# Performance work log

Measured on AMD Instinct MI355X. Metric: run time of the kernel, lower is better.

## Reference

```python
import jax, jax.numpy as jnp
import numpy as np

N, E, D_IN, HEADS, C = 100000, 1600000, 128, 4, 32  # C = out_channels per head


def setup_inputs() -> dict:
    key = jax.random.key(0)
    ks = jax.random.split(key, 10)
    s = 1.0 / np.sqrt(D_IN)
    return {
        "x": jax.random.normal(ks[0], (N, D_IN), jnp.float32),
        "edge_index": jax.random.randint(ks[1], (2, E), 0, N, jnp.int64),
        "Wq": jax.random.normal(ks[2], (D_IN, HEADS * C), jnp.float32) * s,
        "bq": jnp.zeros((HEADS * C,), jnp.float32),
        "Wk": jax.random.normal(ks[3], (D_IN, HEADS * C), jnp.float32) * s,
        "bk": jnp.zeros((HEADS * C,), jnp.float32),
        "Wv": jax.random.normal(ks[4], (D_IN, HEADS * C), jnp.float32) * s,
        "bv": jnp.zeros((HEADS * C,), jnp.float32),
        "Wskip": jax.random.normal(ks[5], (D_IN, HEADS * C), jnp.float32) * s,
        "bskip": jnp.zeros((HEADS * C,), jnp.float32),
    }


def reference(x, edge_index, Wq, bq, Wk, bk, Wv, bv, Wskip, bskip):
    n = x.shape[0]
    src, dst = edge_index[0], edge_index[1]  # message flows src (j) -> dst (i)
    q = (x @ Wq + bq).reshape(n, HEADS, C)
    k = (x @ Wk + bk).reshape(n, HEADS, C)
    v = (x @ Wv + bv).reshape(n, HEADS, C)

    # per-edge attention logits [E, H]
    alpha = jnp.einsum('ehc,ehc->eh', q[dst], k[src]) / jnp.sqrt(jnp.float32(C))

    # segment softmax over incoming edges of each target node
    m = jax.ops.segment_max(alpha, dst, num_segments=n)          # [N, H]
    p = jnp.exp(alpha - m[dst])                                   # [E, H]
    z = jax.ops.segment_sum(p, dst, num_segments=n)               # [N, H]
    w = p / (z[dst] + 1e-16)                                      # [E, H]

    # softmax-weighted scatter aggregation of values
    out = jax.ops.segment_sum(v[src] * w[:, :, None], dst, num_segments=n)
    out = out.reshape(n, HEADS * C)

    # root/skip connection (beta=False default: plain add)
    out = out + x @ Wskip + bskip
    return out
```

## Files before the change

### kernel.cpp

```cpp
#include <hip/hip_runtime.h>

#define DIN 128
#define NHEADS 4
#define CH 32
#define MT 128
#define NPB 256
#define EPB_IT 25

#define ST_H 136

typedef _Float16 h8 __attribute__((ext_vector_type(8)));
typedef _Float16 h2 __attribute__((ext_vector_type(2)));
typedef float f4 __attribute__((ext_vector_type(4)));

__global__ __launch_bounds__(256) void prep_w(
    const float* __restrict__ Wq, const float* __restrict__ Wk,
    const float* __restrict__ Wv, const float* __restrict__ Wsk,
    _Float16* __restrict__ wt)
{
    int i = blockIdx.x * 256 + threadIdx.x;
    if (i >= 4 * 16384) return;
    int mat = i >> 14;
    int rem = i & 16383;
    int n  = rem >> 7;
    int kk = rem & 127;
    const float* W = (mat == 0) ? Wq : (mat == 1) ? Wk : (mat == 2) ? Wv : Wsk;
    wt[i] = (_Float16)W[kk * 128 + n];
}

__global__ __launch_bounds__(256) void qkvs_mat(
    const float* __restrict__ x, const _Float16* __restrict__ wt,
    const float* __restrict__ bq, const float* __restrict__ bk,
    const float* __restrict__ bv, const float* __restrict__ bsk,
    _Float16* __restrict__ qh, _Float16* __restrict__ kh,
    _Float16* __restrict__ vh, _Float16* __restrict__ skiph, int N)
{
    __shared__ _Float16 Sbuf[17408];
    const int t = threadIdx.x;
    const int mat = blockIdx.x;
    const int rowBase = blockIdx.y * MT;

    for (int i = t; i < MT * 16; i += 256) {
        int r  = i >> 4;
        int c8 = i & 15;
        int gr = rowBase + r;
        _Float16 h[8];
        if (gr < N) {
            float4 f0 = reinterpret_cast<const float4*>(x)[(size_t)gr * 32 + c8 * 2];
            float4 f1 = reinterpret_cast<const float4*>(x)[(size_t)gr * 32 + c8 * 2 + 1];
            h[0] = (_Float16)f0.x; h[1] = (_Float16)f0.y;
            h[2] = (_Float16)f0.z; h[3] = (_Float16)f0.w;
            h[4] = (_Float16)f1.x; h[5] = (_Float16)f1.y;
            h[6] = (_Float16)f1.z; h[7] = (_Float16)f1.w;
        } else {
            #pragma unroll
            for (int j = 0; j < 8; ++j) h[j] = (_Float16)0.f;
        }
        *reinterpret_cast<uint4*>(&Sbuf[r * 128 + ((c8 ^ (r & 7)) << 3)]) =
            *reinterpret_cast<uint4*>(h);
    }
    __syncthreads();

    const int wid  = t >> 6;
    const int l    = t & 63;
    const int lm   = l & 15;
    const int quad = l >> 4;

    const _Float16* __restrict__ Bsrc = wt + (size_t)mat * 16384;

    f4 acc[2][8];
    #pragma unroll
    for (int ms = 0; ms < 2; ++ms)
        #pragma unroll
        for (int nt = 0; nt < 8; ++nt)
            acc[ms][nt] = (f4){0.f, 0.f, 0.f, 0.f};

    #pragma unroll
    for (int kq = 0; kq < 4; ++kq) {
        const int c8 = kq * 4 + quad;
        const int k0 = c8 << 3;
        h8 a0 = *reinterpret_cast<const h8*>(
            &Sbuf[(wid * 32 + lm) * 128 + ((c8 ^ (lm & 7)) << 3)]);
        h8 a1 = *reinterpret_cast<const h8*>(
            &Sbuf[(wid * 32 + 16 + lm) * 128 + ((c8 ^ (lm & 7)) << 3)]);
        #pragma unroll
        for (int nt = 0; nt < 8; ++nt) {
            h8 b = *reinterpret_cast<const h8*>(
                &Bsrc[(size_t)(nt * 16 + lm) * 128 + k0]);
            acc[0][nt] = __builtin_amdgcn_mfma_f32_16x16x32_f16(a0, b, acc[0][nt], 0, 0, 0);
            acc[1][nt] = __builtin_amdgcn_mfma_f32_16x16x32_f16(a1, b, acc[1][nt], 0, 0, 0);
        }
    }
    __syncthreads();

    const float* bias = (mat == 0) ? bq : (mat == 1) ? bk : (mat == 2) ? bv : bsk;

    #pragma unroll
    for (int ms = 0; ms < 2; ++ms) {
        #pragma unroll
        for (int nt = 0; nt < 8; ++nt) {
            int col = nt * 16 + lm;
            float bsv = bias[col];
            int row = wid * 32 + ms * 16 + quad * 4;
            #pragma unroll
            for (int i2 = 0; i2 < 4; ++i2)
                Sbuf[(row + i2) * ST_H + col] = (_Float16)(acc[ms][nt][i2] + bsv);
        }
    }
    __syncthreads();

    _Float16* __restrict__ dst = (mat == 0) ? qh : (mat == 1) ? kh
                               : (mat == 2) ? vh : skiph;
    for (int j = t; j < 2048; j += 256) {
        int r  = j >> 4;
        int c0 = (j & 15) << 3;
        int gr = rowBase + r;
        if (gr < N)
            *reinterpret_cast<uint4*>(&dst[(size_t)gr * 128 + c0]) =
                *reinterpret_cast<const uint4*>(&Sbuf[r * ST_H + c0]);
    }
}

__global__ __launch_bounds__(256) void bucket_hist(
    const int* __restrict__ ei, int* __restrict__ bcnt, int E, int nb)
{
    __shared__ int lds[512];
    for (int b = threadIdx.x; b < nb; b += 256) lds[b] = 0;
    __syncthreads();
    for (long long i = (long long)blockIdx.x * 256 + threadIdx.x; i < E;
         i += (long long)gridDim.x * 256)
        atomicAdd(&lds[ei[(size_t)E + i] >> 8], 1);
    __syncthreads();
    for (int b = threadIdx.x; b < nb; b += 256)
        if (lds[b]) atomicAdd(&bcnt[b], lds[b]);
}

__global__ __launch_bounds__(512) void scan_buckets(
    const int* __restrict__ bcnt, int* __restrict__ boff,
    int* __restrict__ bcur, int nb)
{
    __shared__ int ws[8];
    int t = threadIdx.x, lane = t & 63, wid = t >> 6;
    int v = (t < nb) ? bcnt[t] : 0;
    int s = v;
    #pragma unroll
    for (int off = 1; off < 64; off <<= 1) {
        int n = __shfl_up(s, off);
        if (lane >= off) s += n;
    }
    if (lane == 63) ws[wid] = s;
    __syncthreads();
    int add = 0;
    for (int w = 0; w < wid; ++w) add += ws[w];
    int excl = s - v + add;
    if (t < nb) { boff[t] = excl; bcur[t] = excl; }
    if (t == nb - 1) boff[nb] = excl + v;
}

__global__ __launch_bounds__(256) void bucket_scatter(
    const int* __restrict__ ei, int* __restrict__ bcur,
    unsigned* __restrict__ pairs, int E, int nb)
{
    __shared__ int cnt[512];
    int t = threadIdx.x;
    for (int b = t; b < nb; b += 256) cnt[b] = 0;
    __syncthreads();

    long long e0 = (long long)blockIdx.x * (256 * EPB_IT);
    int ps[EPB_IT], pd[EPB_IT];
    #pragma unroll
    for (int j = 0; j < EPB_IT; ++j) {
        long long e = e0 + j * 256 + t;
        if (e < E) {
            ps[j] = ei[e];
            pd[j] = ei[(size_t)E + e];
            atomicAdd(&cnt[pd[j] >> 8], 1);
        } else pd[j] = -1;
    }
    __syncthreads();
    for (int b = t; b < nb; b += 256) {
        int c = cnt[b];
        if (c) cnt[b] = atomicAdd(&bcur[b], c);
    }
    __syncthreads();
    #pragma unroll
    for (int j = 0; j < EPB_IT; ++j) {
        if (pd[j] >= 0) {
            int pos = atomicAdd(&cnt[pd[j] >> 8], 1);
            pairs[pos] = ((unsigned)ps[j] << 8) | ((unsigned)pd[j] & 255u);
        }
    }
}

__global__ __launch_bounds__(256) void bucket_finalize(
    const unsigned* __restrict__ pairs, const int* __restrict__ boff,
    int* __restrict__ rowptr, int* __restrict__ sorted, int N, int nb)
{
    __shared__ int cnt[NPB];
    __shared__ int cur[NPB];
    __shared__ int ws[4];
    int b = blockIdx.x, t = threadIdx.x;
    cnt[t] = 0;
    __syncthreads();
    int s0 = boff[b], e0 = boff[b + 1];
    for (int i = s0 + t; i < e0; i += 256)
        atomicAdd(&cnt[pairs[i] & (NPB - 1)], 1);
    __syncthreads();

    int v = cnt[t];
    int lane = t & 63, wid = t >> 6;
    int incl = v;
    #pragma unroll
    for (int off = 1; off < 64; off <<= 1) {
        int n = __shfl_up(incl, off);
        if (lane >= off) incl += n;
    }
    if (lane == 63) ws[wid] = incl;
    __syncthreads();
    int add = 0;
    for (int w = 0; w < wid; ++w) add += ws[w];
    int base = s0 + (incl - v) + add;

    int node = b * NPB + t;
    if (node < N) rowptr[node] = base;
    if (b == nb - 1 && t == 0) rowptr[N] = boff[nb];
    cur[t] = base;
    __syncthreads();

    for (int i = s0 + t; i < e0; i += 256) {
        unsigned pr = pairs[i];
        int pos = atomicAdd(&cur[pr & (NPB - 1)], 1);
        sorted[pos] = (int)(pr >> 8);
    }
}

__device__ inline float4 cvt4(unsigned lo, unsigned hi) {
    union { unsigned u[2]; _Float16 h[4]; } c;
    c.u[0] = lo; c.u[1] = hi;
    return make_float4((float)c.h[0], (float)c.h[1], (float)c.h[2], (float)c.h[3]);
}

__device__ inline h2 as_h2(unsigned u) {
    union { unsigned u; h2 h; } c;
    c.u = u;
    return c.h;
}

__global__ __launch_bounds__(256) void node_aggregate(
    const _Float16* __restrict__ q, const _Float16* __restrict__ kh,
    const _Float16* __restrict__ vh, const _Float16* __restrict__ skiph,
    const int* __restrict__ rowptr, const int* __restrict__ srcs,
    float* __restrict__ out, int N)
{
    int gid  = blockIdx.x * 256 + threadIdx.x;
    int node = gid >> 5;
    if (node >= N) return;
    int l = gid & 31;

    uint2 qu = reinterpret_cast<const uint2*>(q + (size_t)node * 128)[l];
    h2 qa = as_h2(qu.x), qb = as_h2(qu.y);

    float4 acc = make_float4(0.f, 0.f, 0.f, 0.f);
    float z = 0.f;

    const uint2* k2 = reinterpret_cast<const uint2*>(kh);
    const uint2* v2 = reinterpret_cast<const uint2*>(vh);
    const float SC = 0.17677669529663687f;
    int e0 = rowptr[node], e1 = rowptr[node + 1];
    int e = e0;

    for (; e + 8 <= e1; e += 8) {
        int s[8];
        #pragma unroll
        for (int j = 0; j < 8; ++j) s[j] = srcs[e + j];
        uint2 kr[8], vr[8];
        #pragma unroll
        for (int j = 0; j < 8; ++j) kr[j] = k2[(size_t)s[j] * 32 + l];
        #pragma unroll
        for (int j = 0; j < 8; ++j) vr[j] = v2[(size_t)s[j] * 32 + l];

        float sv[8];
        #pragma unroll
        for (int j = 0; j < 8; ++j) {
            sv[j] = __builtin_amdgcn_fdot2(qa, as_h2(kr[j].x),
                    __builtin_amdgcn_fdot2(qb, as_h2(kr[j].y), 0.f, false), false);
        }
        #pragma unroll
        for (int j = 0; j < 8; ++j) sv[j] += __shfl_xor(sv[j], 1);
        #pragma unroll
        for (int j = 0; j < 8; ++j) sv[j] += __shfl_xor(sv[j], 2);
        #pragma unroll
        for (int j = 0; j < 8; ++j) sv[j] += __shfl_xor(sv[j], 4);

        #pragma unroll
        for (int j = 0; j < 8; ++j) {
            float p = __expf(sv[j] * SC);
            float4 v = cvt4(vr[j].x, vr[j].y);
            z += p;
            acc.x += p * v.x; acc.y += p * v.y;
            acc.z += p * v.z; acc.w += p * v.w;
        }
    }
    for (; e < e1; ++e) {
        int s0 = srcs[e];
        uint2 kr = k2[(size_t)s0 * 32 + l];
        uint2 vr = v2[(size_t)s0 * 32 + l];
        float sa = __builtin_amdgcn_fdot2(qa, as_h2(kr.x),
                   __builtin_amdgcn_fdot2(qb, as_h2(kr.y), 0.f, false), false);
        sa += __shfl_xor(sa, 1);
        sa += __shfl_xor(sa, 2);
        sa += __shfl_xor(sa, 4);
        float pa = __expf(sa * SC);
        float4 v0 = cvt4(vr.x, vr.y);
        z += pa;
        acc.x += pa * v0.x; acc.y += pa * v0.y;
        acc.z += pa * v0.z; acc.w += pa * v0.w;
    }

    uint2 su = reinterpret_cast<const uint2*>(skiph + (size_t)node * 128)[l];
    float4 sk = cvt4(su.x, su.y);
    float inv = 1.f / (z + 1e-16f);
    float4 o;
    o.x = sk.x + acc.x * inv; o.y = sk.y + acc.y * inv;
    o.z = sk.z + acc.z * inv; o.w = sk.w + acc.w * inv;
    reinterpret_cast<float4*>(out)[(size_t)node * 32 + l] = o;
}

extern "C" void kernel_launch(void* const* d_in, const int* in_sizes, int n_in,
                              void* d_out, int out_size, void* d_ws, size_t ws_size,
                              hipStream_t stream)
{
    const float* x   = (const float*)d_in[0];
    const int*   ei  = (const int*)d_in[1];
    const float* Wq  = (const float*)d_in[2];
    const float* bq  = (const float*)d_in[3];
    const float* Wk  = (const float*)d_in[4];
    const float* bk  = (const float*)d_in[5];
    const float* Wv  = (const float*)d_in[6];
    const float* bv  = (const float*)d_in[7];
    const float* Wsk = (const float*)d_in[8];
    const float* bsk = (const float*)d_in[9];
    float* out = (float*)d_out;

    const int N = in_sizes[0] / DIN;
    const int E = in_sizes[1] / 2;
    const int nb = (N + NPB - 1) / NPB;

    _Float16* qh    = (_Float16*)d_ws;
    _Float16* kh    = qh + (size_t)N * DIN;
    _Float16* vh    = kh + (size_t)N * DIN;
    _Float16* skiph = vh + (size_t)N * DIN;
    _Float16* wt    = skiph + (size_t)N * DIN;
    unsigned* pairs = (unsigned*)(wt + 4 * 16384);
    int* sorted   = (int*)(pairs + (size_t)E);
    int* rowptr   = sorted + E;
    int* bcnt     = rowptr + (N + 1);
    int* boff     = bcnt + 512;
    int* bcur     = boff + 513;

    hipMemsetAsync(bcnt, 0, 512 * sizeof(int), stream);

    prep_w<<<(4 * 16384 + 255) / 256, 256, 0, stream>>>(Wq, Wk, Wv, Wsk, wt);

    dim3 ggrid(4, (N + MT - 1) / MT);
    qkvs_mat<<<ggrid, 256, 0, stream>>>(x, wt, bq, bk, bv, bsk,
                                        qh, kh, vh, skiph, N);

    bucket_hist<<<256, 256, 0, stream>>>(ei, bcnt, E, nb);
    scan_buckets<<<1, 512, 0, stream>>>(bcnt, boff, bcur, nb);
    int sb = (E + 256 * EPB_IT - 1) / (256 * EPB_IT);
    bucket_scatter<<<sb, 256, 0, stream>>>(ei, bcur, pairs, E, nb);
    bucket_finalize<<<nb, 256, 0, stream>>>(pairs, boff, rowptr, sorted, N, nb);

    int ab = (N * 32 + 255) / 256;
    node_aggregate<<<ab, 256, 0, stream>>>(qh, kh, vh, skiph, rowptr, sorted, out, N);
}
```

Measured before the change: 401.9 us.

## Halve GEMM row tile and stage bucket scatter through shared memory

```diff
diff --git a/kernel.cpp b/kernel.cpp
--- a/kernel.cpp
+++ b/kernel.cpp
@@ -3,9 +3,10 @@
 #define DIN 128
 #define NHEADS 4
 #define CH 32
-#define MT 128
+#define MT 64
 #define NPB 256
 #define EPB_IT 25
+#define FB_CAP 6144
 
 #define ST_H 136
 
@@ -35,7 +36,7 @@
     _Float16* __restrict__ qh, _Float16* __restrict__ kh,
     _Float16* __restrict__ vh, _Float16* __restrict__ skiph, int N)
 {
-    __shared__ _Float16 Sbuf[17408];
+    __shared__ _Float16 Sbuf[MT * ST_H];
     const int t = threadIdx.x;
     const int mat = blockIdx.x;
     const int rowBase = blockIdx.y * MT;
@@ -68,27 +69,22 @@
 
     const _Float16* __restrict__ Bsrc = wt + (size_t)mat * 16384;
 
-    f4 acc[2][8];
-    #pragma unroll
-    for (int ms = 0; ms < 2; ++ms)
-        #pragma unroll
-        for (int nt = 0; nt < 8; ++nt)
-            acc[ms][nt] = (f4){0.f, 0.f, 0.f, 0.f};
+    f4 acc[8];
+    #pragma unroll
+    for (int nt = 0; nt < 8; ++nt)
+        acc[nt] = (f4){0.f, 0.f, 0.f, 0.f};
 
     #pragma unroll
     for (int kq = 0; kq < 4; ++kq) {
         const int c8 = kq * 4 + quad;
         const int k0 = c8 << 3;
         h8 a0 = *reinterpret_cast<const h8*>(
-            &Sbuf[(wid * 32 + lm) * 128 + ((c8 ^ (lm & 7)) << 3)]);
-        h8 a1 = *reinterpret_cast<const h8*>(
-            &Sbuf[(wid * 32 + 16 + lm) * 128 + ((c8 ^ (lm & 7)) << 3)]);
+            &Sbuf[(wid * 16 + lm) * 128 + ((c8 ^ (lm & 7)) << 3)]);
         #pragma unroll
         for (int nt = 0; nt < 8; ++nt) {
             h8 b = *reinterpret_cast<const h8*>(
                 &Bsrc[(size_t)(nt * 16 + lm) * 128 + k0]);
-            acc[0][nt] = __builtin_amdgcn_mfma_f32_16x16x32_f16(a0, b, acc[0][nt], 0, 0, 0);
-            acc[1][nt] = __builtin_amdgcn_mfma_f32_16x16x32_f16(a1, b, acc[1][nt], 0, 0, 0);
+            acc[nt] = __builtin_amdgcn_mfma_f32_16x16x32_f16(a0, b, acc[nt], 0, 0, 0);
         }
     }
     __syncthreads();
@@ -96,22 +92,19 @@
     const float* bias = (mat == 0) ? bq : (mat == 1) ? bk : (mat == 2) ? bv : bsk;
 
     #pragma unroll
-    for (int ms = 0; ms < 2; ++ms) {
-        #pragma unroll
-        for (int nt = 0; nt < 8; ++nt) {
-            int col = nt * 16 + lm;
-            float bsv = bias[col];
-            int row = wid * 32 + ms * 16 + quad * 4;
-            #pragma unroll
-            for (int i2 = 0; i2 < 4; ++i2)
-                Sbuf[(row + i2) * ST_H + col] = (_Float16)(acc[ms][nt][i2] + bsv);
-        }
+    for (int nt = 0; nt < 8; ++nt) {
+        int col = nt * 16 + lm;
+        float bsv = bias[col];
+        int row = wid * 16 + quad * 4;
+        #pragma unroll
+        for (int i2 = 0; i2 < 4; ++i2)
+            Sbuf[(row + i2) * ST_H + col] = (_Float16)(acc[nt][i2] + bsv);
     }
     __syncthreads();
 
     _Float16* __restrict__ dst = (mat == 0) ? qh : (mat == 1) ? kh
                                : (mat == 2) ? vh : skiph;
-    for (int j = t; j < 2048; j += 256) {
+    for (int j = t; j < MT * 16; j += 256) {
         int r  = j >> 4;
         int c0 = (j & 15) << 3;
         int gr = rowBase + r;
@@ -199,10 +192,12 @@
     __shared__ int cnt[NPB];
     __shared__ int cur[NPB];
     __shared__ int ws[4];
+    __shared__ int sbuf[FB_CAP];
     int b = blockIdx.x, t = threadIdx.x;
     cnt[t] = 0;
     __syncthreads();
     int s0 = boff[b], e0 = boff[b + 1];
+    int sz = e0 - s0;
     for (int i = s0 + t; i < e0; i += 256)
         atomicAdd(&cnt[pairs[i] & (NPB - 1)], 1);
     __syncthreads();
@@ -219,18 +214,29 @@
     __syncthreads();
     int add = 0;
     for (int w = 0; w < wid; ++w) add += ws[w];
-    int base = s0 + (incl - v) + add;
+    int lbase = (incl - v) + add;
 
     int node = b * NPB + t;
-    if (node < N) rowptr[node] = base;
+    if (node < N) rowptr[node] = s0 + lbase;
     if (b == nb - 1 && t == 0) rowptr[N] = boff[nb];
-    cur[t] = base;
-    __syncthreads();
-
-    for (int i = s0 + t; i < e0; i += 256) {
-        unsigned pr = pairs[i];
-        int pos = atomicAdd(&cur[pr & (NPB - 1)], 1);
-        sorted[pos] = (int)(pr >> 8);
+    cur[t] = lbase;
+    __syncthreads();
+
+    if (sz <= FB_CAP) {
+        for (int i = s0 + t; i < e0; i += 256) {
+            unsigned pr = pairs[i];
+            int lpos = atomicAdd(&cur[pr & (NPB - 1)], 1);
+            sbuf[lpos] = (int)(pr >> 8);
+        }
+        __syncthreads();
+        for (int i = t; i < sz; i += 256)
+            sorted[s0 + i] = sbuf[i];
+    } else {
+        for (int i = s0 + t; i < e0; i += 256) {
+            unsigned pr = pairs[i];
+            int pos = atomicAdd(&cur[pr & (NPB - 1)], 1);
+            sorted[s0 + pos] = (int)(pr >> 8);
+        }
     }
 }
 
```

After: 404.4 us. About the same (+0.6%).
